# Kernel optimization log

Measured on AMD Instinct MI355X. Metric: run time of the kernel, lower is better.

Reference implementation:

```python
import jax, jax.numpy as jnp
import numpy as np
import math

B, L, D, H = 2, 2048, 2048, 16
DK = D // H  # 128

def _rope_tables(dim, max_len, base=10000.0):
    freqs = 1.0 / (base ** (np.arange(0, dim, 2, dtype=np.float32) / dim))
    t = np.arange(max_len, dtype=np.float32)
    ang = np.outer(t, freqs)  # [max_len, dim//2]
    return jnp.asarray(np.cos(ang)), jnp.asarray(np.sin(ang))

def setup_inputs() -> dict:
    key = jax.random.key(0)
    kx, kq, ko = jax.random.split(key, 3)
    x = jax.random.normal(kx, (B, L, D), dtype=jnp.float32)
    w_qkv = jax.random.normal(kq, (D, 3 * D), dtype=jnp.float32) * 0.02
    w_o = jax.random.normal(ko, (D, D), dtype=jnp.float32) * 0.02
    cos, sin = _rope_tables(DK, L)
    return {"x": x, "w_qkv": w_qkv, "w_o": w_o, "cos": cos, "sin": sin}

def _apply_rope(t, cos, sin):
    # t: [B, H, L, DK]; cos/sin: [L, DK//2]
    d2 = t.shape[-1] // 2
    t1, t2 = t[..., :d2], t[..., d2:]
    c = cos[None, None, :, :]
    s = sin[None, None, :, :]
    return jnp.concatenate([t1 * c - t2 * s, t1 * s + t2 * c], axis=-1)

def reference(x, w_qkv, w_o, cos, sin):
    b, l, d = x.shape
    qkv = (x @ w_qkv).reshape(b, l, 3, H, DK)
    q = jnp.transpose(qkv[:, :, 0], (0, 2, 1, 3))  # [B,H,L,DK]
    k = jnp.transpose(qkv[:, :, 1], (0, 2, 1, 3))
    v = jnp.transpose(qkv[:, :, 2], (0, 2, 1, 3))
    q = _apply_rope(q, cos[:l], sin[:l])
    k = _apply_rope(k, cos[:l], sin[:l])
    scores = jnp.einsum('bhqd,bhkd->bhqk', q, k) / math.sqrt(DK)
    causal = jnp.triu(jnp.ones((l, l), dtype=bool), k=1)  # total_len - L + 1 = 1
    scores = jnp.where(causal[None, None], -jnp.inf, scores)
    attn = jax.nn.softmax(scores, axis=-1)  # dropout p=0 -> identity
    out = jnp.einsum('bhqk,bhkd->bhqd', attn, v)
    out = jnp.transpose(out, (0, 2, 1, 3)).reshape(b, l, d)
    return out @ w_o, k, v
```

## Files before the change

kernel.cpp:

```cpp
#include <hip/hip_runtime.h>
#include <hip/hip_bf16.h>

#define NB 2
#define NL 2048
#define ND 2048
#define NH 16
#define NDK 128
#define SCALE 0.08838834764831845f

#define AS1 __attribute__((address_space(1)))
#define AS3 __attribute__((address_space(3)))

typedef __attribute__((ext_vector_type(8))) __bf16 bf16x8;
typedef __attribute__((ext_vector_type(4))) float f32x4;

__device__ __forceinline__ unsigned short f2bf(float f) {
    union { float f; unsigned u; } v; v.f = f;
    return (unsigned short)((v.u + 0x7fffu + ((v.u >> 16) & 1u)) >> 16);
}
__device__ __forceinline__ float bf2f(unsigned short h) {
    union { unsigned u; float f; } v; v.u = ((unsigned)h) << 16;
    return v.f;
}

__global__ __launch_bounds__(256)
void convert_bf16_kernel(const float* __restrict__ in, unsigned short* __restrict__ outp)
{
    int i = blockIdx.x * 256 + threadIdx.x;
    const float4 a = ((const float4*)in)[2 * i];
    const float4 b = ((const float4*)in)[2 * i + 1];
    unsigned short t[8] = { f2bf(a.x), f2bf(a.y), f2bf(a.z), f2bf(a.w),
                            f2bf(b.x), f2bf(b.y), f2bf(b.z), f2bf(b.w) };
    ((uint4*)outp)[i] = *(uint4*)t;
}

__global__ __launch_bounds__(256)
void transpose_convert_kernel(const float* __restrict__ in, unsigned short* __restrict__ outp,
                              int R, int C)
{
    __shared__ float T[64][65];
    const int tr0 = blockIdx.y * 64;
    const int tc0 = blockIdx.x * 64;
    const int t = threadIdx.x;
    const int r = t >> 2;
    const int q = t & 3;
    const float* src = in + (size_t)(tr0 + r) * C + tc0 + q * 16;
    #pragma unroll
    for (int i = 0; i < 4; i++) {
        float4 f = *(const float4*)(src + 4 * i);
        T[r][q * 16 + 4 * i + 0] = f.x;
        T[r][q * 16 + 4 * i + 1] = f.y;
        T[r][q * 16 + 4 * i + 2] = f.z;
        T[r][q * 16 + 4 * i + 3] = f.w;
    }
    __syncthreads();
    unsigned short tmp[16];
    #pragma unroll
    for (int i = 0; i < 16; i++) tmp[i] = f2bf(T[q * 16 + i][r]);
    unsigned short* dst = outp + (size_t)(tc0 + r) * R + tr0 + q * 16;
    *(uint4*)dst       = *(uint4*)&tmp[0];
    *(uint4*)(dst + 8) = *(uint4*)&tmp[8];
}

__global__ __launch_bounds__(256)
void transpose_v_kernel(const float* __restrict__ v, unsigned short* __restrict__ vt)
{
    __shared__ float T[64][65];
    const int bh = blockIdx.z;
    const int l0 = blockIdx.y * 64;
    const int d0 = blockIdx.x * 64;
    const int t = threadIdx.x;
    const int r = t >> 2;
    const int q = t & 3;
    const float* src = v + (size_t)bh * NL * NDK + (size_t)(l0 + r) * NDK + d0 + q * 16;
    #pragma unroll
    for (int i = 0; i < 4; i++) {
        float4 f = *(const float4*)(src + 4 * i);
        T[r][q * 16 + 4 * i + 0] = f.x;
        T[r][q * 16 + 4 * i + 1] = f.y;
        T[r][q * 16 + 4 * i + 2] = f.z;
        T[r][q * 16 + 4 * i + 3] = f.w;
    }
    __syncthreads();
    unsigned short tmp[16];
    #pragma unroll
    for (int i = 0; i < 16; i++) tmp[i] = f2bf(T[q * 16 + i][r]);
    unsigned short* dst = vt + (size_t)bh * NDK * NL + (size_t)(d0 + r) * NL + l0 + q * 16;
    *(uint4*)dst       = *(uint4*)&tmp[0];
    *(uint4*)(dst + 8) = *(uint4*)&tmp[8];
}

template<int EPI>
__global__ __launch_bounds__(256)
void gemm_bf16(const unsigned short* __restrict__ A, const unsigned short* __restrict__ Bt,
               float* __restrict__ y_dst,
               unsigned short* __restrict__ q_raw,
               float* __restrict__ k_dst, float* __restrict__ v_dst,
               int K, int NT)
{
    __shared__ __align__(16) unsigned short As[3][128][32];
    __shared__ __align__(16) unsigned short Bs[3][128][32];

    const int tid = threadIdx.x;
    const int lane = tid & 63;
    const int l16 = lane & 15, g = lane >> 4;
    const int w = tid >> 6;
    const int wr = w >> 1, wc = w & 1;

    const int cpn = NT >> 3;
    const int bid = blockIdx.x;
    const int xcd = bid & 7, local = bid >> 3;
    const int bx = xcd * cpn + local % cpn;
    const int by = local / cpn;
    const int m0 = by * 128, n0 = bx * 128;

    const int rowl = (w << 4) + (lane >> 2);
    const int swl = (rowl >> 1) & 3;
    const int kofl = ((lane & 3) ^ swl) << 3;
    const unsigned short* gA = A + (size_t)(m0 + rowl) * K + kofl;
    const unsigned short* gB = Bt + (size_t)(n0 + rowl) * K + kofl;
    const int ldsoff = (w << 10) + (lane << 4);

    f32x4 acc[4][4] = {};
    const int NTILES = K >> 5;

    auto STAGE = [&](int t, int buf) {
        const int k0 = t << 5;
        char* baseA = (char*)&As[buf][0][0] + ldsoff;
        char* baseB = (char*)&Bs[buf][0][0] + ldsoff;
        #pragma unroll
        for (int i = 0; i < 2; i++) {
            __builtin_amdgcn_global_load_lds((const AS1 void*)(gA + (size_t)i * 64 * K + k0),
                                             (AS3 void*)(baseA + i * 4096), 16, 0, 0);
            __builtin_amdgcn_global_load_lds((const AS1 void*)(gB + (size_t)i * 64 * K + k0),
                                             (AS3 void*)(baseB + i * 4096), 16, 0, 0);
        }
    };

    const int rsw = (l16 >> 1) & 3;

    STAGE(0, 0); STAGE(1, 1);

    int bufC = 0;
    for (int t = 0; t < NTILES; t++) {
        const int bufS = (bufC == 0) ? 2 : bufC - 1;
        if (t + 2 < NTILES) STAGE(t + 2, bufS);
        if (t + 2 < NTILES)      asm volatile("s_waitcnt vmcnt(8)" ::: "memory");
        else if (t + 1 < NTILES) asm volatile("s_waitcnt vmcnt(4)" ::: "memory");
        else                     asm volatile("s_waitcnt vmcnt(0)" ::: "memory");
        __builtin_amdgcn_s_barrier();
        __builtin_amdgcn_sched_barrier(0);

        const char* pa = (const char*)&As[bufC][0][0];
        const char* pb = (const char*)&Bs[bufC][0][0];
        bf16x8 af[4], bfr[4];
        #pragma unroll
        for (int r = 0; r < 4; r++) {
            int row = wr * 64 + r * 16 + l16;
            af[r] = *(const bf16x8*)(pa + row * 64 + ((g ^ rsw) << 4));
        }
        #pragma unroll
        for (int c = 0; c < 4; c++) {
            int row = wc * 64 + c * 16 + l16;
            bfr[c] = *(const bf16x8*)(pb + row * 64 + ((g ^ rsw) << 4));
        }
        #pragma unroll
        for (int r = 0; r < 4; r++)
            #pragma unroll
            for (int c = 0; c < 4; c++)
                acc[r][c] = __builtin_amdgcn_mfma_f32_16x16x32_bf16(af[r], bfr[c], acc[r][c], 0, 0, 0);

        __builtin_amdgcn_s_barrier();
        __builtin_amdgcn_sched_barrier(0);
        bufC = (bufC == 2) ? 0 : bufC + 1;
    }

    if constexpr (EPI == 0) {
        const int m3 = bx >> 4, h = bx & 15;
        #pragma unroll
        for (int r = 0; r < 4; r++) {
            int mrow = m0 + wr * 64 + r * 16 + g * 4;
            int b = mrow >> 11, l = mrow & 2047;
            size_t rb = ((size_t)(b * NH + h) * NL + l) * NDK;
            #pragma unroll
            for (int c = 0; c < 4; c++) {
                int dk = wc * 64 + c * 16 + l16;
                #pragma unroll
                for (int i = 0; i < 4; i++) {
                    float val = acc[r][c][i];
                    size_t off = rb + (size_t)i * NDK + dk;
                    if (m3 == 0) q_raw[off] = f2bf(val);
                    else if (m3 == 1) k_dst[off] = val;
                    else v_dst[off] = val;
                }
            }
        }
    } else {
        #pragma unroll
        for (int r = 0; r < 4; r++) {
            int mrow = m0 + wr * 64 + r * 16 + g * 4;
            #pragma unroll
            for (int c = 0; c < 4; c++) {
                int ncol = n0 + wc * 64 + c * 16 + l16;
                #pragma unroll
                for (int i = 0; i < 4; i++)
                    y_dst[(size_t)(mrow + i) * ND + ncol] = acc[r][c][i];
            }
        }
    }
}

__global__ __launch_bounds__(256)
void rope_k_kernel(float* __restrict__ kp, unsigned short* __restrict__ k_bf,
                   const float* __restrict__ ct, const float* __restrict__ st)
{
    int idx = blockIdx.x * 256 + threadIdx.x;
    int d = idx & 63;
    int rr = idx >> 6;
    size_t ro = (size_t)rr * NDK;
    int l = rr & (NL - 1);
    float c = ct[l * 64 + d], s = st[l * 64 + d];
    float t1 = kp[ro + d], t2 = kp[ro + d + 64];
    float o1 = t1 * c - t2 * s, o2 = t1 * s + t2 * c;
    kp[ro + d] = o1; kp[ro + d + 64] = o2;
    k_bf[ro + d]      = f2bf(o1);
    k_bf[ro + d + 64] = f2bf(o2);
}

__global__ __launch_bounds__(256)
void attn_kernel(const unsigned short* __restrict__ q,
                 const unsigned short* __restrict__ k,
                 const unsigned short* __restrict__ vt,
                 unsigned short* __restrict__ attn_out,
                 const float* __restrict__ ct, const float* __restrict__ st)
{
    __shared__ __align__(16) unsigned short Ks[64][128];
    __shared__ __align__(16) unsigned short Vts[128][64];
    __shared__ __align__(16) unsigned short Ps[4][16][64];

    char* const ksb = (char*)&Ks[0][0];
    char* const vsb = (char*)&Vts[0][0];
    char* const psb = (char*)&Ps[0][0][0];

    const int tid = threadIdx.x, lane = tid & 63, w = tid >> 6;
    const int l16 = lane & 15, g = lane >> 4;
    const int bh = blockIdx.x;
    const int b = bh >> 4, h = bh & 15;
    const size_t base = (size_t)bh * NL * NDK;

    const int krow = tid >> 2;
    const int kq = tid & 3;
    const int kwb = krow * 256 + kq * 64;
    const int kwx = (krow & 7) << 4;
    const int vrow = tid >> 1;
    const int vh = tid & 1;
    const int vwb = vrow * 128 + vh * 64;
    const int vwx = (vrow & 7) << 4;

    const int rdx = (l16 & 7) << 4;

    const unsigned short* const kbase = k + base + (size_t)krow * NDK + kq * 32;
    const unsigned short* const vbase = vt + base + (size_t)vrow * NL + vh * 32;

    for (int half = 0; half < 2; half++) {
        const int jq = half ? (int)blockIdx.y : 31 - (int)blockIdx.y;
        const int qb = jq * 64;

        bf16x8 aq[4];
        {
            const int l = qb + w * 16 + l16;
            const unsigned short* src = q + base + (size_t)l * NDK + g * 8;
            union { bf16x8 v; unsigned short s[8]; } raw[4], outv[4];
            #pragma unroll
            for (int ks2 = 0; ks2 < 4; ks2++) raw[ks2].v = *(const bf16x8*)(src + ks2 * 32);
            const float* cb = ct + (size_t)l * 64 + g * 8;
            const float* sb = st + (size_t)l * 64 + g * 8;
            float cv[2][8], sv2[2][8];
            #pragma unroll
            for (int hh = 0; hh < 2; hh++) {
                float4 c0 = *(const float4*)(cb + 32 * hh);
                float4 c1 = *(const float4*)(cb + 32 * hh + 4);
                float4 s0 = *(const float4*)(sb + 32 * hh);
                float4 s1 = *(const float4*)(sb + 32 * hh + 4);
                cv[hh][0]=c0.x; cv[hh][1]=c0.y; cv[hh][2]=c0.z; cv[hh][3]=c0.w;
                cv[hh][4]=c1.x; cv[hh][5]=c1.y; cv[hh][6]=c1.z; cv[hh][7]=c1.w;
                sv2[hh][0]=s0.x; sv2[hh][1]=s0.y; sv2[hh][2]=s0.z; sv2[hh][3]=s0.w;
                sv2[hh][4]=s1.x; sv2[hh][5]=s1.y; sv2[hh][6]=s1.z; sv2[hh][7]=s1.w;
            }
            #pragma unroll
            for (int hh = 0; hh < 2; hh++)
                #pragma unroll
                for (int j = 0; j < 8; j++) {
                    float t1 = bf2f(raw[hh].s[j]), t2 = bf2f(raw[hh + 2].s[j]);
                    float c = cv[hh][j], s = sv2[hh][j];
                    outv[hh].s[j]     = f2bf(t1 * c - t2 * s);
                    outv[hh + 2].s[j] = f2bf(t1 * s + t2 * c);
                }
            #pragma unroll
            for (int ks2 = 0; ks2 < 4; ks2++) aq[ks2] = outv[ks2].v;
        }

        f32x4 o[8] = {};
        float m_r[4], lv[4];
        #pragma unroll
        for (int i = 0; i < 4; i++) { m_r[i] = -1e30f; lv[i] = 0.f; }

        uint4 pk0, pk1, pk2, pk3, pv0, pv1, pv2, pv3;
        {
            const unsigned short* ks = kbase;
            pk0 = *(const uint4*)(ks);
            pk1 = *(const uint4*)(ks + 8);
            pk2 = *(const uint4*)(ks + 16);
            pk3 = *(const uint4*)(ks + 24);
            const unsigned short* vs = vbase;
            pv0 = *(const uint4*)(vs);
            pv1 = *(const uint4*)(vs + 8);
            pv2 = *(const uint4*)(vs + 16);
            pv3 = *(const uint4*)(vs + 24);
        }

        for (int kv0 = 0; kv0 <= qb; kv0 += 64) {
            __syncthreads();
            *(uint4*)(ksb + ((kwb     ) ^ kwx)) = pk0;
            *(uint4*)(ksb + ((kwb + 16) ^ kwx)) = pk1;
            *(uint4*)(ksb + ((kwb + 32) ^ kwx)) = pk2;
            *(uint4*)(ksb + ((kwb + 48) ^ kwx)) = pk3;
            *(uint4*)(vsb + ((vwb     ) ^ vwx)) = pv0;
            *(uint4*)(vsb + ((vwb + 16) ^ vwx)) = pv1;
            *(uint4*)(vsb + ((vwb + 32) ^ vwx)) = pv2;
            *(uint4*)(vsb + ((vwb + 48) ^ vwx)) = pv3;
            __syncthreads();

            if (kv0 + 64 <= qb) {
                const unsigned short* ks = kbase + (size_t)(kv0 + 64) * NDK;
                pk0 = *(const uint4*)(ks);
                pk1 = *(const uint4*)(ks + 8);
                pk2 = *(const uint4*)(ks + 16);
                pk3 = *(const uint4*)(ks + 24);
                const unsigned short* vs = vbase + kv0 + 64;
                pv0 = *(const uint4*)(vs);
                pv1 = *(const uint4*)(vs + 8);
                pv2 = *(const uint4*)(vs + 16);
                pv3 = *(const uint4*)(vs + 24);
                __builtin_amdgcn_sched_barrier(0);
            }

            f32x4 sv[4];
            __builtin_amdgcn_s_setprio(1);
            #pragma unroll
            for (int cf = 0; cf < 4; cf++) {
                const int krb = (cf * 16 + l16) * 256 + g * 16;
                f32x4 a = {};
                #pragma unroll
                for (int ks2 = 0; ks2 < 4; ks2++) {
                    bf16x8 kf = *(const bf16x8*)(ksb + ((krb + 64 * ks2) ^ rdx));
                    a = __builtin_amdgcn_mfma_f32_16x16x32_bf16(aq[ks2], kf, a, 0, 0, 0);
                }
                sv[cf] = a;
            }
            __builtin_amdgcn_s_setprio(0);

            const int kvl = kv0 + l16;
            const int rowb = qb + w * 16 + g * 4;
            #pragma unroll
            for (int i = 0; i < 4; i++) {
                int row = rowb + i;
                float s0 = sv[0][i] * SCALE;
                float s1 = sv[1][i] * SCALE;
                float s2 = sv[2][i] * SCALE;
                float s3 = sv[3][i] * SCALE;
                if (kvl      > row) s0 = -1e30f;
                if (kvl + 16 > row) s1 = -1e30f;
                if (kvl + 32 > row) s2 = -1e30f;
                if (kvl + 48 > row) s3 = -1e30f;
                float mx = fmaxf(fmaxf(s0, s1), fmaxf(s2, s3));
                mx = fmaxf(mx, __shfl_xor(mx, 1));
                mx = fmaxf(mx, __shfl_xor(mx, 2));
                mx = fmaxf(mx, __shfl_xor(mx, 4));
                mx = fmaxf(mx, __shfl_xor(mx, 8));
                float mnew = fmaxf(m_r[i], mx);
                float fac = __expf(m_r[i] - mnew);
                float p0 = __expf(s0 - mnew);
                float p1 = __expf(s1 - mnew);
                float p2 = __expf(s2 - mnew);
                float p3 = __expf(s3 - mnew);
                lv[i] = lv[i] * fac + ((p0 + p1) + (p2 + p3));
                m_r[i] = mnew;
                #pragma unroll
                for (int c8 = 0; c8 < 8; c8++) o[c8][i] *= fac;
                const int pr = g * 4 + i;
                char* pw = psb + w * 2048 + pr * 128;
                const int px = (pr & 7) << 4;
                const int cb2 = l16 << 1;
                *(unsigned short*)(pw + ((cb2)      ^ px)) = f2bf(p0);
                *(unsigned short*)(pw + ((cb2 + 32) ^ px)) = f2bf(p1);
                *(unsigned short*)(pw + ((cb2 + 64) ^ px)) = f2bf(p2);
                *(unsigned short*)(pw + ((cb2 + 96) ^ px)) = f2bf(p3);
            }
            asm volatile("s_waitcnt lgkmcnt(0)" ::: "memory");
            __builtin_amdgcn_sched_barrier(0);

            bf16x8 pf[2];
            #pragma unroll
            for (int kc = 0; kc < 2; kc++)
                pf[kc] = *(const bf16x8*)(psb + w * 2048 + l16 * 128 + ((kc * 64 + g * 16) ^ rdx));
            __builtin_amdgcn_s_setprio(1);
            #pragma unroll
            for (int c8 = 0; c8 < 8; c8++) {
                const int vrb = (c8 * 16 + l16) * 128 + g * 16;
                #pragma unroll
                for (int kc = 0; kc < 2; kc++) {
                    bf16x8 vf = *(const bf16x8*)(vsb + ((vrb + kc * 64) ^ rdx));
                    o[c8] = __builtin_amdgcn_mfma_f32_16x16x32_bf16(pf[kc], vf, o[c8], 0, 0, 0);
                }
            }
            __builtin_amdgcn_s_setprio(0);
        }

        #pragma unroll
        for (int i = 0; i < 4; i++) {
            float ls = lv[i];
            ls += __shfl_xor(ls, 1);
            ls += __shfl_xor(ls, 2);
            ls += __shfl_xor(ls, 4);
            ls += __shfl_xor(ls, 8);
            float inv = 1.0f / ls;
            int qrow = qb + w * 16 + g * 4 + i;
            size_t rb = ((size_t)(b * NL + qrow)) * ND + h * NDK;
            #pragma unroll
            for (int c8 = 0; c8 < 8; c8++)
                attn_out[rb + c8 * 16 + l16] = f2bf(o[c8][i] * inv);
        }
    }
}

__global__ void ws_signature_kernel(float* y) { if (threadIdx.x == 0) y[0] = 12345.0f; }

extern "C" void kernel_launch(void* const* d_in, const int* in_sizes, int n_in,
                              void* d_out, int out_size, void* d_ws, size_t ws_size,
                              hipStream_t stream)
{
    const float* x     = (const float*)d_in[0];
    const float* w_qkv = (const float*)d_in[1];
    const float* w_o   = (const float*)d_in[2];
    const float* ct    = (const float*)d_in[3];
    const float* st    = (const float*)d_in[4];

    const size_t NTOK = (size_t)NB * NL * ND;
    float* y_out = (float*)d_out;
    float* k_out = y_out + NTOK;
    float* v_out = y_out + 2 * NTOK;

    const size_t need = (6 * NTOK + 4 * (size_t)ND * ND) * sizeof(unsigned short);
    if (ws_size < need) {
        ws_signature_kernel<<<1, 64, 0, stream>>>(y_out);
        return;
    }
    unsigned short* x_bf  = (unsigned short*)d_ws;
    unsigned short* Wt    = x_bf + NTOK;
    unsigned short* Wt_o  = Wt + (size_t)3 * ND * ND;
    unsigned short* q_raw = Wt_o + (size_t)ND * ND;
    unsigned short* q_bf  = q_raw + NTOK;
    unsigned short* k_bf  = q_bf + NTOK;
    unsigned short* Vt    = k_bf + NTOK;
    unsigned short* a_bf  = Vt + NTOK;

    convert_bf16_kernel<<<4096, 256, 0, stream>>>(x, x_bf);
    transpose_convert_kernel<<<dim3(96, 32), 256, 0, stream>>>(w_qkv, Wt, ND, 3 * ND);
    transpose_convert_kernel<<<dim3(32, 32), 256, 0, stream>>>(w_o, Wt_o, ND, ND);
    gemm_bf16<0><<<1536, 256, 0, stream>>>(x_bf, Wt, nullptr, q_raw, k_out, v_out, ND, 48);
    rope_k_kernel<<<16384, 256, 0, stream>>>(k_out, k_bf, ct, st);
    transpose_v_kernel<<<dim3(2, 32, 32), 256, 0, stream>>>(v_out, Vt);
    attn_kernel<<<dim3(32, 16), 256, 0, stream>>>(q_raw, k_bf, Vt, a_bf, ct, st);
    gemm_bf16<1><<<512, 256, 0, stream>>>(a_bf, Wt_o, y_out, nullptr, nullptr, nullptr, ND, 16);
}
```

Before: 318.1 us.

## Replace GEMM with 128x256-tile, 512-thread kernel using K=64 double-buffered stages

Both projection GEMMs now use a new kernel with 128x256 output tiles, 8 waves per block, and K-step 64. Loads are double-buffered and interleaved with split MFMA phases, with s_setprio raised around the MFMA groups and an XOR swizzle on LDS rows. The larger tile raises arithmetic intensity and halves the block count. The trade-offs are more LDS per block, fewer blocks for the output-projection GEMM (256), and a more fragile hand-scheduled wait/barrier sequence.

```diff
diff --git a/kernel.cpp b/kernel.cpp
--- a/kernel.cpp
+++ b/kernel.cpp
@@ -91,120 +91,174 @@
 }
 
 template<int EPI>
-__global__ __launch_bounds__(256)
-void gemm_bf16(const unsigned short* __restrict__ A, const unsigned short* __restrict__ Bt,
-               float* __restrict__ y_dst,
-               unsigned short* __restrict__ q_raw,
-               float* __restrict__ k_dst, float* __restrict__ v_dst,
-               int K, int NT)
-{
-    __shared__ __align__(16) unsigned short As[3][128][32];
-    __shared__ __align__(16) unsigned short Bs[3][128][32];
+__global__ __launch_bounds__(512, 2)
+void gemm256(const unsigned short* __restrict__ A, const unsigned short* __restrict__ Bt,
+             float* __restrict__ y_dst,
+             unsigned short* __restrict__ q_raw,
+             float* __restrict__ k_dst, float* __restrict__ v_dst,
+             int K, int NTB)
+{
+    __shared__ __align__(16) unsigned short As[2][128][64];
+    __shared__ __align__(16) unsigned short Bs[2][256][64];
 
     const int tid = threadIdx.x;
     const int lane = tid & 63;
+    const int w = tid >> 6;
+    const int wr = w >> 2, wc = w & 3;
     const int l16 = lane & 15, g = lane >> 4;
-    const int w = tid >> 6;
-    const int wr = w >> 1, wc = w & 1;
-
-    const int cpn = NT >> 3;
+
+    const int cpn = NTB >> 3 ? NTB >> 3 : 1;
     const int bid = blockIdx.x;
-    const int xcd = bid & 7, local = bid >> 3;
-    const int bx = xcd * cpn + local % cpn;
-    const int by = local / cpn;
-    const int m0 = by * 128, n0 = bx * 128;
-
-    const int rowl = (w << 4) + (lane >> 2);
-    const int swl = (rowl >> 1) & 3;
-    const int kofl = ((lane & 3) ^ swl) << 3;
-    const unsigned short* gA = A + (size_t)(m0 + rowl) * K + kofl;
-    const unsigned short* gB = Bt + (size_t)(n0 + rowl) * K + kofl;
-    const int ldsoff = (w << 10) + (lane << 4);
+    int bx, by;
+    if (NTB >= 8) {
+        const int xcd = bid & 7, local = bid >> 3;
+        bx = xcd * (NTB >> 3) + local % (NTB >> 3);
+        by = local / (NTB >> 3);
+    } else {
+        bx = bid % NTB;
+        by = bid / NTB;
+    }
+    (void)cpn;
+    const int m0 = by * 128, n0 = bx * 256;
+
+    char* const asb = (char*)&As[0][0][0];
+    char* const bsb = (char*)&Bs[0][0][0];
+
+    const int srow = w * 16 + (lane >> 3);
+    const int swz  = ((lane & 7) ^ (lane >> 3)) << 3;
+    const unsigned short* const gA0 = A  + (size_t)(m0 + srow) * K + swz;
+    const unsigned short* const gB0 = Bt + (size_t)(n0 + srow) * K + swz;
+    const int sdst = srow * 128 + ((lane & 7) << 4);
+
+    auto STA = [&](int buf, int k0) {
+        const unsigned short* s = gA0 + k0;
+        char* d = asb + buf * 16384 + sdst;
+        __builtin_amdgcn_global_load_lds((const AS1 void*)(s),         (AS3 void*)(d),        16, 0, 0);
+        __builtin_amdgcn_global_load_lds((const AS1 void*)(s + 8 * K), (AS3 void*)(d + 1024), 16, 0, 0);
+    };
+    auto STB = [&](int buf, int R0, int k0) {
+        const unsigned short* s = gB0 + (size_t)R0 * K + k0;
+        char* d = bsb + buf * 32768 + R0 * 128 + sdst;
+        __builtin_amdgcn_global_load_lds((const AS1 void*)(s),         (AS3 void*)(d),        16, 0, 0);
+        __builtin_amdgcn_global_load_lds((const AS1 void*)(s + 8 * K), (AS3 void*)(d + 1024), 16, 0, 0);
+    };
+
+    const int xr = l16 & 7;
+    const int aRow = (wr * 64 + l16) * 128;
+    const int bRow = (wc * 64 + l16) * 128;
+    const int cp0 = ((0 + g) ^ xr) << 4;
+    const int cp1 = ((4 + g) ^ xr) << 4;
 
     f32x4 acc[4][4] = {};
-    const int NTILES = K >> 5;
-
-    auto STAGE = [&](int t, int buf) {
-        const int k0 = t << 5;
-        char* baseA = (char*)&As[buf][0][0] + ldsoff;
-        char* baseB = (char*)&Bs[buf][0][0] + ldsoff;
-        #pragma unroll
-        for (int i = 0; i < 2; i++) {
-            __builtin_amdgcn_global_load_lds((const AS1 void*)(gA + (size_t)i * 64 * K + k0),
-                                             (AS3 void*)(baseA + i * 4096), 16, 0, 0);
-            __builtin_amdgcn_global_load_lds((const AS1 void*)(gB + (size_t)i * 64 * K + k0),
-                                             (AS3 void*)(baseB + i * 4096), 16, 0, 0);
-        }
-    };
-
-    const int rsw = (l16 >> 1) & 3;
-
-    STAGE(0, 0); STAGE(1, 1);
-
-    int bufC = 0;
-    for (int t = 0; t < NTILES; t++) {
-        const int bufS = (bufC == 0) ? 2 : bufC - 1;
-        if (t + 2 < NTILES) STAGE(t + 2, bufS);
-        if (t + 2 < NTILES)      asm volatile("s_waitcnt vmcnt(8)" ::: "memory");
-        else if (t + 1 < NTILES) asm volatile("s_waitcnt vmcnt(4)" ::: "memory");
-        else                     asm volatile("s_waitcnt vmcnt(0)" ::: "memory");
+    bf16x8 af[4][2], bfr[4][2];
+
+    auto LDA4 = [&](int buf) {
+        const char* p = asb + buf * 16384 + aRow;
+        #pragma unroll
+        for (int f = 0; f < 4; f++) {
+            af[f][0] = *(const bf16x8*)(p + f * 2048 + cp0);
+            af[f][1] = *(const bf16x8*)(p + f * 2048 + cp1);
+        }
+    };
+    auto LDB2 = [&](int buf, int f0) {
+        const char* p = bsb + buf * 32768 + bRow + f0 * 2048;
+        #pragma unroll
+        for (int f = 0; f < 2; f++) {
+            bfr[f0 + f][0] = *(const bf16x8*)(p + f * 2048 + cp0);
+            bfr[f0 + f][1] = *(const bf16x8*)(p + f * 2048 + cp1);
+        }
+    };
+    auto MM16 = [&](int nf0) {
+        __builtin_amdgcn_s_setprio(1);
+        #pragma unroll
+        for (int mf = 0; mf < 4; mf++)
+            #pragma unroll
+            for (int nf = 0; nf < 2; nf++) {
+                f32x4 c = acc[mf][nf0 + nf];
+                c = __builtin_amdgcn_mfma_f32_16x16x32_bf16(af[mf][0], bfr[nf0 + nf][0], c, 0, 0, 0);
+                c = __builtin_amdgcn_mfma_f32_16x16x32_bf16(af[mf][1], bfr[nf0 + nf][1], c, 0, 0, 0);
+                acc[mf][nf0 + nf] = c;
+            }
+        __builtin_amdgcn_s_setprio(0);
+    };
+    auto PH_TOP = [&]() {
+        __builtin_amdgcn_s_barrier();
+        asm volatile("s_waitcnt lgkmcnt(0)" ::: "memory");
+        __builtin_amdgcn_sched_barrier(0);
+    };
+    auto PH_END = [&]() {
         __builtin_amdgcn_s_barrier();
         __builtin_amdgcn_sched_barrier(0);
-
-        const char* pa = (const char*)&As[bufC][0][0];
-        const char* pb = (const char*)&Bs[bufC][0][0];
-        bf16x8 af[4], bfr[4];
-        #pragma unroll
-        for (int r = 0; r < 4; r++) {
-            int row = wr * 64 + r * 16 + l16;
-            af[r] = *(const bf16x8*)(pa + row * 64 + ((g ^ rsw) << 4));
-        }
-        #pragma unroll
-        for (int c = 0; c < 4; c++) {
-            int row = wc * 64 + c * 16 + l16;
-            bfr[c] = *(const bf16x8*)(pb + row * 64 + ((g ^ rsw) << 4));
-        }
-        #pragma unroll
-        for (int r = 0; r < 4; r++)
-            #pragma unroll
-            for (int c = 0; c < 4; c++)
-                acc[r][c] = __builtin_amdgcn_mfma_f32_16x16x32_bf16(af[r], bfr[c], acc[r][c], 0, 0, 0);
-
-        __builtin_amdgcn_s_barrier();
+    };
+
+    auto ITER = [&](bool full, int kb1, int kn) {
+        LDA4(0); LDB2(0, 0);
+        STB(1, 0, kb1); STB(1, 128, kb1);
+        PH_TOP(); MM16(0); PH_END();
+        LDB2(0, 2);
+        if (full) STA(0, kn);
+        PH_TOP(); MM16(2);
+        if (full) asm volatile("s_waitcnt vmcnt(2)" ::: "memory");
+        else      asm volatile("s_waitcnt vmcnt(0)" ::: "memory");
         __builtin_amdgcn_sched_barrier(0);
-        bufC = (bufC == 2) ? 0 : bufC + 1;
-    }
+        PH_END();
+        LDA4(1); LDB2(1, 0);
+        if (full) { STB(0, 0, kn); STB(0, 128, kn); }
+        PH_TOP(); MM16(0); PH_END();
+        LDB2(1, 2);
+        if (full) STA(1, kn + 64);
+        PH_TOP(); MM16(2);
+        if (full) {
+            asm volatile("s_waitcnt vmcnt(2)" ::: "memory");
+            __builtin_amdgcn_sched_barrier(0);
+        }
+        PH_END();
+    };
+
+    STA(0, 0);
+    STB(0, 0, 0); STB(0, 128, 0);
+    STA(1, 64);
+    asm volatile("s_waitcnt vmcnt(2)" ::: "memory");
+    __builtin_amdgcn_s_barrier();
+    __builtin_amdgcn_sched_barrier(0);
+
+    const int NI = K >> 7;
+    for (int i = 0; i < NI - 1; i++)
+        ITER(true, i * 128 + 64, i * 128 + 128);
+    ITER(false, (NI - 1) * 128 + 64, 0);
 
     if constexpr (EPI == 0) {
-        const int m3 = bx >> 4, h = bx & 15;
-        #pragma unroll
-        for (int r = 0; r < 4; r++) {
-            int mrow = m0 + wr * 64 + r * 16 + g * 4;
-            int b = mrow >> 11, l = mrow & 2047;
-            size_t rb = ((size_t)(b * NH + h) * NL + l) * NDK;
-            #pragma unroll
-            for (int c = 0; c < 4; c++) {
-                int dk = wc * 64 + c * 16 + l16;
+        #pragma unroll
+        for (int mf = 0; mf < 4; mf++) {
+            const int mrow = m0 + wr * 64 + mf * 16 + g * 4;
+            const int b = mrow >> 11, l = mrow & 2047;
+            #pragma unroll
+            for (int nf = 0; nf < 4; nf++) {
+                const int ncol = n0 + wc * 64 + nf * 16 + l16;
+                const int sec = ncol >> 11;
+                const int dd = ncol & 2047;
+                const int h = dd >> 7, dk = dd & 127;
+                const size_t rb = ((size_t)(b * NH + h) * NL + l) * NDK + dk;
                 #pragma unroll
-                for (int i = 0; i < 4; i++) {
-                    float val = acc[r][c][i];
-                    size_t off = rb + (size_t)i * NDK + dk;
-                    if (m3 == 0) q_raw[off] = f2bf(val);
-                    else if (m3 == 1) k_dst[off] = val;
-                    else v_dst[off] = val;
+                for (int i2 = 0; i2 < 4; i2++) {
+                    const float val = acc[mf][nf][i2];
+                    const size_t off = rb + (size_t)i2 * NDK;
+                    if (sec == 0)      q_raw[off] = f2bf(val);
+                    else if (sec == 1) k_dst[off] = val;
+                    else               v_dst[off] = val;
                 }
             }
         }
     } else {
         #pragma unroll
-        for (int r = 0; r < 4; r++) {
-            int mrow = m0 + wr * 64 + r * 16 + g * 4;
-            #pragma unroll
-            for (int c = 0; c < 4; c++) {
-                int ncol = n0 + wc * 64 + c * 16 + l16;
+        for (int mf = 0; mf < 4; mf++) {
+            const int mrow = m0 + wr * 64 + mf * 16 + g * 4;
+            #pragma unroll
+            for (int nf = 0; nf < 4; nf++) {
+                const int ncol = n0 + wc * 64 + nf * 16 + l16;
                 #pragma unroll
-                for (int i = 0; i < 4; i++)
-                    y_dst[(size_t)(mrow + i) * ND + ncol] = acc[r][c][i];
+                for (int i2 = 0; i2 < 4; i2++)
+                    y_dst[(size_t)(mrow + i2) * ND + ncol] = acc[mf][nf][i2];
             }
         }
     }
@@ -468,9 +522,9 @@
     convert_bf16_kernel<<<4096, 256, 0, stream>>>(x, x_bf);
     transpose_convert_kernel<<<dim3(96, 32), 256, 0, stream>>>(w_qkv, Wt, ND, 3 * ND);
     transpose_convert_kernel<<<dim3(32, 32), 256, 0, stream>>>(w_o, Wt_o, ND, ND);
-    gemm_bf16<0><<<1536, 256, 0, stream>>>(x_bf, Wt, nullptr, q_raw, k_out, v_out, ND, 48);
+    gemm256<0><<<768, 512, 0, stream>>>(x_bf, Wt, nullptr, q_raw, k_out, v_out, ND, 24);
     rope_k_kernel<<<16384, 256, 0, stream>>>(k_out, k_bf, ct, st);
     transpose_v_kernel<<<dim3(2, 32, 32), 256, 0, stream>>>(v_out, Vt);
     attn_kernel<<<dim3(32, 16), 256, 0, stream>>>(q_raw, k_bf, Vt, a_bf, ct, st);
-    gemm_bf16<1><<<512, 256, 0, stream>>>(a_bf, Wt_o, y_out, nullptr, nullptr, nullptr, ND, 16);
-}
+    gemm256<1><<<256, 512, 0, stream>>>(a_bf, Wt_o, y_out, nullptr, nullptr, nullptr, ND, 8);
+}
```

After: 332.9 us. 4.6% more time.
